# Performance work log

Hardware: AMD Instinct MI355X
Metric: run time of the kernel (lower is better)

## Reference

```python
import jax, jax.numpy as jnp
import numpy as np

B, N, IN, HID, OUT = 32, 128, 64, 128, 64
_off = np.ones((N, N)) - np.eye(N)
RECV, SEND = np.where(_off)  # rel_rec one-hot rows -> receiver idx, rel_send -> sender idx
E = N * (N - 1)


def _bn(x, g, b):
    # BatchNorm1d in training mode over flattened (B*M, C), eps=1e-5, biased var
    c = x.shape[-1]
    xf = x.reshape(-1, c)
    m = xf.mean(0)
    v = ((xf - m) ** 2).mean(0)
    return (((xf - m) / jnp.sqrt(v + 1e-5)) * g + b).reshape(x.shape)


def _mlp(x, W1, b1, W2, b2, g, b):
    h = jax.nn.silu(x @ W1 + b1)
    h = jax.nn.silu(h @ W2 + b2)
    return _bn(h, g, b)


def setup_inputs() -> dict:
    key = jax.random.key(0)
    ks = jax.random.split(key, 8)
    p = lambda k, s: jax.random.normal(k, s, dtype=jnp.float32) * 0.05
    return {
        "node_feature": jax.random.normal(ks[0], (B, N, IN), dtype=jnp.float32),
        "nodes_mask": jnp.ones((B, N), dtype=jnp.float32),
        "edges_mask": jnp.ones((B, E), dtype=jnp.float32),
        "eW1": p(ks[1], (2 * IN, HID)), "eb1": jnp.full((HID,), 0.1, jnp.float32),
        "eW2": p(ks[2], (HID, HID)), "eb2": jnp.full((HID,), 0.1, jnp.float32),
        "eg": jnp.ones((HID,), jnp.float32), "ebt": jnp.zeros((HID,), jnp.float32),
        "nW1": p(ks[3], (HID, HID)), "nb1": jnp.full((HID,), 0.1, jnp.float32),
        "nW2": p(ks[4], (HID, HID)), "nb2": jnp.full((HID,), 0.1, jnp.float32),
        "ng": jnp.ones((HID,), jnp.float32), "nbt": jnp.zeros((HID,), jnp.float32),
        "mW1": p(ks[5], (IN + HID, HID)), "mb1": jnp.full((HID,), 0.1, jnp.float32),
        "mW2": p(ks[6], (HID, OUT)), "mb2": jnp.full((OUT,), 0.1, jnp.float32),
        "mg": jnp.ones((OUT,), jnp.float32), "mbt": jnp.zeros((OUT,), jnp.float32),
        "t_nodes": 0, "t_edges": 0,
    }


def reference(node_feature, nodes_mask, edges_mask,
              eW1, eb1, eW2, eb2, eg, ebt,
              nW1, nb1, nW2, nb2, ng, nbt,
              mW1, mb1, mW2, mb2, mg, mbt,
              t_nodes, t_edges):
    # edge_model: rel_send/rel_rec one-hot matmuls == gathers
    senders = node_feature[:, SEND, :]    # [B,E,IN]
    receivers = node_feature[:, RECV, :]  # [B,E,IN]
    ef = jnp.concatenate([senders, receivers], axis=-1)  # [B,E,2*IN]
    # skip_first_edge_type=True, edge_types=2 -> only edge_nn[1], norm=1.0
    em = edges_mask[:, :, None]
    msg = _mlp(ef, eW1, eb1, eW2, eb2, eg, ebt) * em  # [B,E,HID]
    mij = msg / 1.0
    out = mij * em       # attention=False
    mij_m = mij * em
    # node_model: rel_rec.T matmul == scatter-sum over receivers, then / N
    incoming = jnp.zeros((B, N, HID), msg.dtype).at[:, RECV, :].add(out) / N
    incoming = _mlp(incoming, nW1, nb1, nW2, nb2, ng, nbt) * nodes_mask[:, :, None]
    nef = jnp.concatenate([node_feature, incoming], axis=-1)  # [B,N,IN+HID]
    out_node = _mlp(nef, mW1, mb1, mW2, mb2, mg, mbt) * nodes_mask[:, :, None]
    return (out_node, mij_m)
```

## Files before the change

kernel.cpp:

```cpp
#include <hip/hip_runtime.h>
#include <hip/hip_bf16.h>

#define BB    32
#define NNODE 128
#define INF   64
#define HIDF  128
#define OUTF  64
#define EE    (NNODE*(NNODE-1))
#define TILES 127
#define NBLK_EDGE (BB*TILES)
#define ROWS_E 520192.0f
#define ROWS_N 4096.0f
#define OUT0_ELEMS (BB*NNODE*OUTF)
#define H2_ELEMS ((size_t)520192*128)

typedef __bf16 bf16_t;
typedef __bf16 bfrag8 __attribute__((ext_vector_type(8)));
typedef __bf16 bfrag4 __attribute__((ext_vector_type(4)));
typedef float  floatx4 __attribute__((ext_vector_type(4)));

__device__ __forceinline__ float ld_g(const void* p, size_t i, int bf) {
    return bf ? (float)((const bf16_t*)p)[i] : ((const float*)p)[i];
}
__device__ __forceinline__ void st_g(void* p, size_t i, float v, int bf) {
    if (bf) ((bf16_t*)p)[i] = (bf16_t)v; else ((float*)p)[i] = v;
}
__device__ __forceinline__ void* mij_ptr(void* dout, int bf) {
    return bf ? (void*)((bf16_t*)dout + OUT0_ELEMS)
              : (void*)((float*)dout + OUT0_ELEMS);
}
__device__ __forceinline__ float silu_f(float x) {
    return x * __builtin_amdgcn_rcpf(1.0f + __expf(-x));
}

__device__ __forceinline__ int swz_col(int row, int col) {
    return col ^ ((row & 15) << 3);
}

__global__ void k_detect(const unsigned int* __restrict__ eg_words,
                         int* __restrict__ flag, float* __restrict__ totE)
{
    if (threadIdx.x == 0) *flag = (eg_words[0] == 0x3F803F80u) ? 1 : 0;
    if (threadIdx.x < 256) totE[threadIdx.x] = 0.f;
}

__global__ __launch_bounds__(256)
void k_prep(const void* __restrict__ W1g, const void* __restrict__ W2g,
            bf16_t* __restrict__ Wf1, bf16_t* __restrict__ Wf2,
            const int* __restrict__ flagp)
{
    const int bf  = *flagp;
    const int idx = blockIdx.x*256 + threadIdx.x;
    const int mat = idx >> 14;
    const int e   = idx & 16383;
    const int n   = e & 127, k = e >> 7;
    const float v = ld_g(mat ? W2g : W1g, e, bf);
    const int NB = n >> 4, ln = n & 15;
    const int ks = k >> 5, q = (k >> 3) & 3, j = k & 7;
    bf16_t* dst = mat ? Wf2 : Wf1;
    dst[((((NB*4 + ks)*4 + q)*16 + ln) << 3) + j] = (bf16_t)v;
}

__global__ __launch_bounds__(256, 4)
void k_edge_mlp(const void* __restrict__ nf,
                const bf16_t* __restrict__ Wf1, const void* __restrict__ b1g,
                const bf16_t* __restrict__ Wf2, const void* __restrict__ b2g,
                void* __restrict__ dout, bf16_t* __restrict__ h2ws,
                const int* __restrict__ flagp, float* __restrict__ totE,
                int h2mode)
{
    __shared__ __align__(16) bf16_t lA[128*128];
    __shared__ float sSum[128], sQ[128];
    const int bf  = *flagp;
    void* h2out = mij_ptr(dout, bf);
    const int bx   = blockIdx.x;
    const int bIdx = bx / TILES;
    const int t    = bx - bIdx*TILES;
    const int tid  = threadIdx.x;

    if (tid < 128) { sSum[tid] = 0.f; sQ[tid] = 0.f; }

    {
#pragma unroll
        for (int s = 0; s < 8; ++s) {
            const int u = tid + s*256;
            const int m = u >> 4;
            const int c = (u & 15) ^ (m & 15);
            const int eb = t*128 + m;
            const unsigned recv = ((unsigned)eb * 33027u) >> 22;
            const unsigned rr   = (unsigned)eb - recv*127u;
            const unsigned send = rr + (rr >= recv ? 1u : 0u);
            const int node = (c & 8) ? (int)recv : (int)send;
            const int coff = (c & 7) * 8;
            const size_t gi = ((size_t)(bIdx*NNODE + node))*INF + coff;
            if (bf) {
                ((uint4*)lA)[u] = *(const uint4*)((const bf16_t*)nf + gi);
            } else {
                const float4 f0 = *(const float4*)((const float*)nf + gi);
                const float4 f1 = *(const float4*)((const float*)nf + gi + 4);
                bfrag8 v;
                v[0]=(bf16_t)f0.x; v[1]=(bf16_t)f0.y; v[2]=(bf16_t)f0.z; v[3]=(bf16_t)f0.w;
                v[4]=(bf16_t)f1.x; v[5]=(bf16_t)f1.y; v[6]=(bf16_t)f1.z; v[7]=(bf16_t)f1.w;
                *(bfrag8*)(lA + (size_t)u*8) = v;
            }
        }
    }
    __syncthreads();

    const int w  = tid >> 6;
    const int L  = tid & 63;
    const int wr = w >> 1;
    const int wc = w & 1;
    const int q  = L >> 4;
    const int ln = L & 15;

    const floatx4 zero4 = {0.f, 0.f, 0.f, 0.f};
    floatx4 acc[4][4];
#pragma unroll
    for (int mt = 0; mt < 4; ++mt)
#pragma unroll
        for (int nt = 0; nt < 4; ++nt) acc[mt][nt] = zero4;

#pragma unroll
    for (int ks = 0; ks < 4; ++ks) {
        const int kk = ks*32;
        bfrag8 af[4], bv[4];
#pragma unroll
        for (int mt = 0; mt < 4; ++mt) {
            const int R = wr*64 + mt*16 + ln;
            af[mt] = *(const bfrag8*)(lA + R*128 + swz_col(R, kk + q*8));
        }
#pragma unroll
        for (int nt = 0; nt < 4; ++nt)
            bv[nt] = *(const bfrag8*)(Wf1 + ((size_t)((wc*4 + nt)*4 + ks)*64 + L)*8);
#pragma unroll
        for (int mt = 0; mt < 4; ++mt)
#pragma unroll
            for (int nt = 0; nt < 4; ++nt)
                acc[mt][nt] = __builtin_amdgcn_mfma_f32_16x16x32_bf16(
                    af[mt], bv[nt], acc[mt][nt], 0, 0, 0);
    }
    __syncthreads();

#pragma unroll
    for (int nt = 0; nt < 4; ++nt) {
        const int col = wc*64 + nt*16 + ln;
        const float bias = ld_g(b1g, col, bf);
#pragma unroll
        for (int mt = 0; mt < 4; ++mt)
#pragma unroll
            for (int r = 0; r < 4; ++r) {
                const int R = wr*64 + mt*16 + q*4 + r;
                lA[R*128 + swz_col(R, col)] = (bf16_t)silu_f(acc[mt][nt][r] + bias);
            }
    }
    __syncthreads();

#pragma unroll
    for (int mt = 0; mt < 4; ++mt)
#pragma unroll
        for (int nt = 0; nt < 4; ++nt) acc[mt][nt] = zero4;
#pragma unroll
    for (int ks = 0; ks < 4; ++ks) {
        const int kk = ks*32;
        bfrag8 af[4], bv[4];
#pragma unroll
        for (int mt = 0; mt < 4; ++mt) {
            const int R = wr*64 + mt*16 + ln;
            af[mt] = *(const bfrag8*)(lA + R*128 + swz_col(R, kk + q*8));
        }
#pragma unroll
        for (int nt = 0; nt < 4; ++nt)
            bv[nt] = *(const bfrag8*)(Wf2 + ((size_t)((wc*4 + nt)*4 + ks)*64 + L)*8);
#pragma unroll
        for (int mt = 0; mt < 4; ++mt)
#pragma unroll
            for (int nt = 0; nt < 4; ++nt)
                acc[mt][nt] = __builtin_amdgcn_mfma_f32_16x16x32_bf16(
                    af[mt], bv[nt], acc[mt][nt], 0, 0, 0);
    }
    __syncthreads();

#pragma unroll
    for (int nt = 0; nt < 4; ++nt) {
        const int col = wc*64 + nt*16 + ln;
        const float bias = ld_g(b2g, col, bf);
        float cs = 0.f, cq = 0.f;
#pragma unroll
        for (int mt = 0; mt < 4; ++mt)
#pragma unroll
            for (int r = 0; r < 4; ++r) {
                const int R = wr*64 + mt*16 + q*4 + r;
                const float v = silu_f(acc[mt][nt][r] + bias);
                cs += v; cq += v*v;
                lA[R*128 + swz_col(R, col)] = (bf16_t)v;
            }
        cs += __shfl_xor(cs, 16); cs += __shfl_xor(cs, 32);
        cq += __shfl_xor(cq, 16); cq += __shfl_xor(cq, 32);
        if (L < 16) { atomicAdd(&sSum[col], cs); atomicAdd(&sQ[col], cq); }
    }
    __syncthreads();

    {
        const size_t Rbase = ((size_t)bIdx*EE + (size_t)t*128) * 128;
#pragma unroll
        for (int s = 0; s < 8; ++s) {
            const int u = tid + s*256;
            const int m = u >> 4;
            const int c = (u & 15) ^ (m & 15);
            const size_t go = Rbase + (size_t)m*128 + c*8;
            if (h2mode) {
                *(uint4*)(h2ws + go) = ((const uint4*)lA)[u];
            } else if (bf) {
                *(uint4*)((bf16_t*)h2out + go) = ((const uint4*)lA)[u];
            } else {
                const bfrag8 vv = *(const bfrag8*)(lA + (size_t)u*8);
                float4 f0, f1;
                f0.x=(float)vv[0]; f0.y=(float)vv[1]; f0.z=(float)vv[2]; f0.w=(float)vv[3];
                f1.x=(float)vv[4]; f1.y=(float)vv[5]; f1.z=(float)vv[6]; f1.w=(float)vv[7];
                *(float4*)((float*)h2out + go)     = f0;
                *(float4*)((float*)h2out + go + 4) = f1;
            }
        }
        if (tid < 128) {
            atomicAdd(&totE[tid],       sSum[tid]);
            atomicAdd(&totE[128 + tid], sQ[tid]);
        }
    }
}

__global__ void k_finalize_edge(const float* __restrict__ tot,
                                const void* __restrict__ g,
                                const void* __restrict__ bt,
                                float* __restrict__ ab,
                                const int* __restrict__ flagp)
{
    const int bf = *flagp;
    const int c = threadIdx.x;
    const float m = tot[c] / ROWS_E;
    float v = tot[128 + c] / ROWS_E - m*m;
    v = fmaxf(v, 0.f);
    const float a = ld_g(g, c, bf) * rsqrtf(v + 1e-5f);
    ab[c]       = a;
    ab[128 + c] = ld_g(bt, c, bf) - m*a;
}

__global__ __launch_bounds__(256)
void k_bn_scatter(void* __restrict__ dout,
                  const bf16_t* __restrict__ h2ws,
                  const void* __restrict__ emask,
                  const float* __restrict__ ab,
                  float* __restrict__ inc,
                  const int* __restrict__ flagp, int h2mode)
{
    const int bf = *flagp;
    void* mij = mij_ptr(dout, bf);
    const void* h2 = h2mode ? (const void*)h2ws : (const void*)mij;
    const int h2bf = h2mode | bf;
    const int bx = blockIdx.x;
    const int b  = bx >> 7, i = bx & 127;
    const int tid = threadIdx.x;
    const int cg = tid & 15, p = tid >> 4;
    const int c0 = cg*8;
    float al[8], be[8];
#pragma unroll
    for (int j = 0; j < 8; ++j) { al[j] = ab[c0+j]; be[j] = ab[128+c0+j]; }
    const size_t seg = (size_t)b*EE + (size_t)i*127;
    float s[8];
#pragma unroll
    for (int j = 0; j < 8; ++j) s[j] = 0.f;
    for (int e = p; e < 127; e += 16) {
        const float em  = ld_g(emask, seg + e, bf);
        const float em2 = em*em;
        const size_t base = (seg + e)*128 + c0;
        float v[8];
        if (h2bf) {
            const bfrag8 u = *(const bfrag8*)((const bf16_t*)h2 + base);
#pragma unroll
            for (int j = 0; j < 8; ++j) v[j] = (float)u[j];
        } else {
            const float4 f0 = *(const float4*)((const float*)h2 + base);
            const float4 f1 = *(const float4*)((const float*)h2 + base + 4);
            v[0]=f0.x; v[1]=f0.y; v[2]=f0.z; v[3]=f0.w;
            v[4]=f1.x; v[5]=f1.y; v[6]=f1.z; v[7]=f1.w;
        }
#pragma unroll
        for (int j = 0; j < 8; ++j) { v[j] = (v[j]*al[j] + be[j])*em2; s[j] += v[j]; }
        if (bf) {
            bfrag8 u;
#pragma unroll
            for (int j = 0; j < 8; ++j) u[j] = (bf16_t)v[j];
            *(bfrag8*)((bf16_t*)mij + base) = u;
        } else {
            float4 f0, f1;
            f0.x=v[0]; f0.y=v[1]; f0.z=v[2]; f0.w=v[3];
            f1.x=v[4]; f1.y=v[5]; f1.z=v[6]; f1.w=v[7];
            *(float4*)((float*)mij + base)     = f0;
            *(float4*)((float*)mij + base + 4) = f1;
        }
    }
    __shared__ float sm[16][128];
#pragma unroll
    for (int j = 0; j < 8; ++j) sm[p][c0+j] = s[j];
    __syncthreads();
    if (tid < 128) {
        float tsum = 0.f;
#pragma unroll
        for (int wk = 0; wk < 16; ++wk) tsum += sm[wk][tid];
        inc[(size_t)(b*NNODE + i)*HIDF + tid] = tsum * (1.0f/NNODE);
    }
}

__global__ __launch_bounds__(128)
void k_node_mlp(const float* __restrict__ inc,
                const void* __restrict__ W1g, const void* __restrict__ b1g,
                const void* __restrict__ W2g, const void* __restrict__ b2g,
                float* __restrict__ h2n, float* __restrict__ partialN,
                const int* __restrict__ flagp)
{
    const int bf = *flagp;
    __shared__ float x[16][128];
    __shared__ float h[16][128];
    const int bx = blockIdx.x;
    const int tid = threadIdx.x;
    const int r0 = bx*16;
    for (int r = 0; r < 16; ++r) x[r][tid] = inc[(size_t)(r0 + r)*128 + tid];
    __syncthreads();

    float a1[16];
#pragma unroll
    for (int r = 0; r < 16; ++r) a1[r] = 0.f;
#pragma unroll 8
    for (int k = 0; k < 128; ++k) {
        const float wv = ld_g(W1g, k*128 + tid, bf);
#pragma unroll
        for (int r = 0; r < 16; ++r) a1[r] += x[r][k]*wv;
    }
    const float bias1 = ld_g(b1g, tid, bf);
#pragma unroll
    for (int r = 0; r < 16; ++r) h[r][tid] = silu_f(a1[r] + bias1);
    __syncthreads();

    float a2[16];
#pragma unroll
    for (int r = 0; r < 16; ++r) a2[r] = 0.f;
#pragma unroll 8
    for (int k = 0; k < 128; ++k) {
        const float wv = ld_g(W2g, k*128 + tid, bf);
#pragma unroll
        for (int r = 0; r < 16; ++r) a2[r] += h[r][k]*wv;
    }
    const float bias2 = ld_g(b2g, tid, bf);
    float s = 0.f, sq = 0.f;
#pragma unroll
    for (int r = 0; r < 16; ++r) {
        const float v = silu_f(a2[r] + bias2);
        h2n[(size_t)(r0 + r)*128 + tid] = v;
        s += v; sq += v*v;
    }
    partialN[(size_t)bx*256 + tid]       = s;
    partialN[(size_t)bx*256 + 128 + tid] = sq;
}

__global__ void k_finalize_node(const float* __restrict__ p,
                                const void* __restrict__ g,
                                const void* __restrict__ bt,
                                float* __restrict__ ab,
                                const int* __restrict__ flagp)
{
    const int bf = *flagp;
    const int c = threadIdx.x;
    float s = 0.f, qv = 0.f;
#pragma unroll 8
    for (int blk = 0; blk < 256; ++blk) { s += p[blk*256 + c]; qv += p[blk*256 + 128 + c]; }
    const float m = s / ROWS_N;
    float v = qv / ROWS_N - m*m;
    v = fmaxf(v, 0.f);
    const float a = ld_g(g, c, bf) * rsqrtf(v + 1e-5f);
    ab[c]       = a;
    ab[128 + c] = ld_g(bt, c, bf) - m*a;
}

__global__ __launch_bounds__(128)
void k_final_mlp(const void* __restrict__ nf,
                 const float* __restrict__ h2n, const float* __restrict__ abn,
                 const void* __restrict__ nmask,
                 const void* __restrict__ W1g, const void* __restrict__ b1g,
                 const void* __restrict__ W2g, const void* __restrict__ b2g,
                 float* __restrict__ hm, float* __restrict__ partialM,
                 const int* __restrict__ flagp)
{
    const int bf = *flagp;
    __shared__ float x[16][192];
    __shared__ float h[16][128];
    const int bx = blockIdx.x;
    const int tid = threadIdx.x;
    const int r0 = bx*16;
    const float an = abn[tid], bn = abn[128 + tid];
    for (int r = 0; r < 16; ++r) {
        const int row = r0 + r;
        const float mask = ld_g(nmask, row, bf);
        if (tid < 64) x[r][tid] = ld_g(nf, (size_t)row*INF + tid, bf);
        x[r][64 + tid] = (h2n[(size_t)row*128 + tid]*an + bn) * mask;
    }
    __syncthreads();

    float a1[16];
#pragma unroll
    for (int r = 0; r < 16; ++r) a1[r] = 0.f;
#pragma unroll 8
    for (int k = 0; k < 192; ++k) {
        const float wv = ld_g(W1g, k*128 + tid, bf);
#pragma unroll
        for (int r = 0; r < 16; ++r) a1[r] += x[r][k]*wv;
    }
    const float bias1 = ld_g(b1g, tid, bf);
#pragma unroll
    for (int r = 0; r < 16; ++r) h[r][tid] = silu_f(a1[r] + bias1);
    __syncthreads();

    if (tid < 64) {
        float a2[16];
#pragma unroll
        for (int r = 0; r < 16; ++r) a2[r] = 0.f;
#pragma unroll 8
        for (int k = 0; k < 128; ++k) {
            const float wv = ld_g(W2g, k*64 + tid, bf);
#pragma unroll
            for (int r = 0; r < 16; ++r) a2[r] += h[r][k]*wv;
        }
        const float bias2 = ld_g(b2g, tid, bf);
        float s = 0.f, sq = 0.f;
#pragma unroll
        for (int r = 0; r < 16; ++r) {
            const float v = silu_f(a2[r] + bias2);
            hm[(size_t)(r0 + r)*OUTF + tid] = v;
            s += v; sq += v*v;
        }
        partialM[(size_t)bx*128 + tid]      = s;
        partialM[(size_t)bx*128 + 64 + tid] = sq;
    }
}

__global__ void k_finalize_m(const float* __restrict__ p,
                             const void* __restrict__ g,
                             const void* __restrict__ bt,
                             float* __restrict__ ab,
                             const int* __restrict__ flagp)
{
    const int bf = *flagp;
    const int c = threadIdx.x;
    float s = 0.f, qv = 0.f;
#pragma unroll 8
    for (int blk = 0; blk < 256; ++blk) { s += p[blk*128 + c]; qv += p[blk*128 + 64 + c]; }
    const float m = s / ROWS_N;
    float v = qv / ROWS_N - m*m;
    v = fmaxf(v, 0.f);
    const float a = ld_g(g, c, bf) * rsqrtf(v + 1e-5f);
    ab[c]      = a;
    ab[64 + c] = ld_g(bt, c, bf) - m*a;
}

__global__ void k_out_node(const float* __restrict__ hm,
                           const float* __restrict__ abm,
                           const void* __restrict__ nmask,
                           void* __restrict__ dout,
                           const int* __restrict__ flagp)
{
    const int bf = *flagp;
    const int idx = blockIdx.x*256 + threadIdx.x;
    if (idx >= OUT0_ELEMS) return;
    const int c = idx & 63;
    const int row = idx >> 6;
    const float v = (hm[idx]*abm[c] + abm[64 + c]) * ld_g(nmask, row, bf);
    st_g(dout, idx, v, bf);
}

extern "C" void kernel_launch(void* const* d_in, const int* in_sizes, int n_in,
                              void* d_out, int out_size, void* d_ws, size_t ws_size,
                              hipStream_t stream)
{
    const void* nf    = d_in[0];
    const void* nmask = d_in[1];
    const void* emask = d_in[2];
    const void* eW1   = d_in[3];
    const void* eb1   = d_in[4];
    const void* eW2   = d_in[5];
    const void* eb2   = d_in[6];
    const void* eg    = d_in[7];
    const void* ebt   = d_in[8];
    const void* nW1   = d_in[9];
    const void* nb1   = d_in[10];
    const void* nW2   = d_in[11];
    const void* nb2   = d_in[12];
    const void* ng    = d_in[13];
    const void* nbt   = d_in[14];
    const void* mW1   = d_in[15];
    const void* mb1   = d_in[16];
    const void* mW2   = d_in[17];
    const void* mb2   = d_in[18];
    const void* mg    = d_in[19];
    const void* mbt   = d_in[20];

    float* W    = (float*)d_ws;
    int*   flag = (int*)W;
    float* totE = W    + 64;
    float* abE  = totE + 256;
    float* inc  = abE  + 256;
    float* h2n  = inc  + 524288;
    float* pN   = h2n  + 524288;
    float* abN  = pN   + 65536;
    float* hm   = abN  + 256;
    float* pM   = hm   + 262144;
    float* abM  = pM   + 32768;
    bf16_t* Wf1 = (bf16_t*)(abM + 128);
    bf16_t* Wf2 = Wf1 + 16384;
    bf16_t* h2ws = Wf2 + 16384;

    const size_t base_bytes = (size_t)((char*)h2ws - (char*)d_ws);
    const int h2mode = (ws_size >= base_bytes + H2_ELEMS*2 + 256) ? 1 : 0;

    k_detect<<<dim3(1), dim3(256), 0, stream>>>((const unsigned int*)eg, flag, totE);
    k_prep<<<dim3(128), dim3(256), 0, stream>>>(eW1, eW2, Wf1, Wf2, flag);
    k_edge_mlp<<<dim3(NBLK_EDGE), dim3(256), 0, stream>>>(nf, Wf1, eb1, Wf2, eb2, d_out, h2ws, flag, totE, h2mode);
    k_finalize_edge<<<dim3(1), dim3(128), 0, stream>>>(totE, eg, ebt, abE, flag);
    k_bn_scatter<<<dim3(BB*NNODE), dim3(256), 0, stream>>>(d_out, h2ws, emask, abE, inc, flag, h2mode);
    k_node_mlp<<<dim3(256), dim3(128), 0, stream>>>(inc, nW1, nb1, nW2, nb2, h2n, pN, flag);
    k_finalize_node<<<dim3(1), dim3(128), 0, stream>>>(pN, ng, nbt, abN, flag);
    k_final_mlp<<<dim3(256), dim3(128), 0, stream>>>(nf, h2n, abN, nmask, mW1, mb1, mW2, mb2, hm, pM, flag);
    k_finalize_m<<<dim3(1), dim3(64), 0, stream>>>(pM, mg, mbt, abM, flag);
    k_out_node<<<dim3(1024), dim3(256), 0, stream>>>(hm, abM, nmask, d_out, flag);
}
```

Before: 630.6 us.

## Factor first edge layer into per-node sender/receiver projections

```diff
diff --git a/kernel.cpp b/kernel.cpp
--- a/kernel.cpp
+++ b/kernel.cpp
@@ -16,7 +16,6 @@
 
 typedef __bf16 bf16_t;
 typedef __bf16 bfrag8 __attribute__((ext_vector_type(8)));
-typedef __bf16 bfrag4 __attribute__((ext_vector_type(4)));
 typedef float  floatx4 __attribute__((ext_vector_type(4)));
 
 __device__ __forceinline__ float ld_g(const void* p, size_t i, int bf) {
@@ -33,23 +32,24 @@
     return x * __builtin_amdgcn_rcpf(1.0f + __expf(-x));
 }
 
-__device__ __forceinline__ int swz_col(int row, int col) {
+__device__ __forceinline__ int swz_col(int row, int col)  {
     return col ^ ((row & 15) << 3);
 }
-
-__global__ void k_detect(const unsigned int* __restrict__ eg_words,
-                         int* __restrict__ flag, float* __restrict__ totE)
-{
-    if (threadIdx.x == 0) *flag = (eg_words[0] == 0x3F803F80u) ? 1 : 0;
-    if (threadIdx.x < 256) totE[threadIdx.x] = 0.f;
+__device__ __forceinline__ int swz64_col(int row, int col) {
+    return col ^ ((row & 7) << 3);
 }
 
 __global__ __launch_bounds__(256)
-void k_prep(const void* __restrict__ W1g, const void* __restrict__ W2g,
+void k_prep(const unsigned int* __restrict__ eg_words,
+            const void* __restrict__ W1g, const void* __restrict__ W2g,
             bf16_t* __restrict__ Wf1, bf16_t* __restrict__ Wf2,
-            const int* __restrict__ flagp)
-{
-    const int bf  = *flagp;
+            int* __restrict__ flag, float* __restrict__ totE)
+{
+    const int bf = (eg_words[0] == 0x3F803F80u) ? 1 : 0;
+    if (blockIdx.x == 0) {
+        if (threadIdx.x == 0) *flag = bf;
+        totE[threadIdx.x] = 0.f;
+    }
     const int idx = blockIdx.x*256 + threadIdx.x;
     const int mat = idx >> 14;
     const int e   = idx & 16383;
@@ -61,9 +61,91 @@
     dst[((((NB*4 + ks)*4 + q)*16 + ln) << 3) + j] = (bf16_t)v;
 }
 
+__global__ __launch_bounds__(256)
+void k_sr(const void* __restrict__ nf,
+          const bf16_t* __restrict__ Wf1, const void* __restrict__ b1g,
+          float* __restrict__ Sbuf, float* __restrict__ Rbuf,
+          const int* __restrict__ flagp)
+{
+    __shared__ __align__(16) bf16_t lA[128*64];
+    const int bf  = *flagp;
+    const int r0  = blockIdx.x * 128;
+    const int tid = threadIdx.x;
+
+#pragma unroll
+    for (int s = 0; s < 4; ++s) {
+        const int u = tid + s*256;
+        const int m = u >> 3;
+        const int c = (u & 7) ^ (m & 7);
+        const size_t gi = (size_t)(r0 + m)*INF + c*8;
+        if (bf) {
+            ((uint4*)lA)[u] = *(const uint4*)((const bf16_t*)nf + gi);
+        } else {
+            const float4 f0 = *(const float4*)((const float*)nf + gi);
+            const float4 f1 = *(const float4*)((const float*)nf + gi + 4);
+            bfrag8 v;
+            v[0]=(bf16_t)f0.x; v[1]=(bf16_t)f0.y; v[2]=(bf16_t)f0.z; v[3]=(bf16_t)f0.w;
+            v[4]=(bf16_t)f1.x; v[5]=(bf16_t)f1.y; v[6]=(bf16_t)f1.z; v[7]=(bf16_t)f1.w;
+            *(bfrag8*)(lA + (size_t)u*8) = v;
+        }
+    }
+    __syncthreads();
+
+    const int w  = tid >> 6;
+    const int L  = tid & 63;
+    const int wr = w >> 1;
+    const int wc = w & 1;
+    const int q  = L >> 4;
+    const int ln = L & 15;
+
+    const floatx4 zero4 = {0.f, 0.f, 0.f, 0.f};
+    floatx4 accS[4][4], accR[4][4];
+#pragma unroll
+    for (int mt = 0; mt < 4; ++mt)
+#pragma unroll
+        for (int nt = 0; nt < 4; ++nt) { accS[mt][nt] = zero4; accR[mt][nt] = zero4; }
+
+#pragma unroll
+    for (int ks = 0; ks < 2; ++ks) {
+        bfrag8 af[4], bs[4], br[4];
+#pragma unroll
+        for (int mt = 0; mt < 4; ++mt) {
+            const int Rr = wr*64 + mt*16 + ln;
+            af[mt] = *(const bfrag8*)(lA + Rr*64 + swz64_col(Rr, ks*32 + q*8));
+        }
+#pragma unroll
+        for (int nt = 0; nt < 4; ++nt) {
+            bs[nt] = *(const bfrag8*)(Wf1 + ((size_t)((wc*4 + nt)*4 + ks)*64 + L)*8);
+            br[nt] = *(const bfrag8*)(Wf1 + ((size_t)((wc*4 + nt)*4 + ks + 2)*64 + L)*8);
+        }
+#pragma unroll
+        for (int mt = 0; mt < 4; ++mt)
+#pragma unroll
+            for (int nt = 0; nt < 4; ++nt) {
+                accS[mt][nt] = __builtin_amdgcn_mfma_f32_16x16x32_bf16(
+                    af[mt], bs[nt], accS[mt][nt], 0, 0, 0);
+                accR[mt][nt] = __builtin_amdgcn_mfma_f32_16x16x32_bf16(
+                    af[mt], br[nt], accR[mt][nt], 0, 0, 0);
+            }
+    }
+
+#pragma unroll
+    for (int nt = 0; nt < 4; ++nt) {
+        const int col = wc*64 + nt*16 + ln;
+        const float bias = ld_g(b1g, col, bf);
+#pragma unroll
+        for (int mt = 0; mt < 4; ++mt)
+#pragma unroll
+            for (int r = 0; r < 4; ++r) {
+                const int row = wr*64 + mt*16 + q*4 + r;
+                Sbuf[(size_t)(r0 + row)*128 + col] = accS[mt][nt][r] + bias;
+                Rbuf[(size_t)(r0 + row)*128 + col] = accR[mt][nt][r];
+            }
+    }
+}
+
 __global__ __launch_bounds__(256, 4)
-void k_edge_mlp(const void* __restrict__ nf,
-                const bf16_t* __restrict__ Wf1, const void* __restrict__ b1g,
+void k_edge_mlp(const float* __restrict__ Sbuf, const float* __restrict__ Rbuf,
                 const bf16_t* __restrict__ Wf2, const void* __restrict__ b2g,
                 void* __restrict__ dout, bf16_t* __restrict__ h2ws,
                 const int* __restrict__ flagp, float* __restrict__ totE,
@@ -81,6 +163,7 @@
     if (tid < 128) { sSum[tid] = 0.f; sQ[tid] = 0.f; }
 
     {
+        const size_t nodeBase = (size_t)bIdx*NNODE*128;
 #pragma unroll
         for (int s = 0; s < 8; ++s) {
             const int u = tid + s*256;
@@ -90,19 +173,18 @@
             const unsigned recv = ((unsigned)eb * 33027u) >> 22;
             const unsigned rr   = (unsigned)eb - recv*127u;
             const unsigned send = rr + (rr >= recv ? 1u : 0u);
-            const int node = (c & 8) ? (int)recv : (int)send;
-            const int coff = (c & 7) * 8;
-            const size_t gi = ((size_t)(bIdx*NNODE + node))*INF + coff;
-            if (bf) {
-                ((uint4*)lA)[u] = *(const uint4*)((const bf16_t*)nf + gi);
-            } else {
-                const float4 f0 = *(const float4*)((const float*)nf + gi);
-                const float4 f1 = *(const float4*)((const float*)nf + gi + 4);
-                bfrag8 v;
-                v[0]=(bf16_t)f0.x; v[1]=(bf16_t)f0.y; v[2]=(bf16_t)f0.z; v[3]=(bf16_t)f0.w;
-                v[4]=(bf16_t)f1.x; v[5]=(bf16_t)f1.y; v[6]=(bf16_t)f1.z; v[7]=(bf16_t)f1.w;
-                *(bfrag8*)(lA + (size_t)u*8) = v;
-            }
+            const float* Sp = Sbuf + nodeBase + (size_t)send*128 + c*8;
+            const float* Rp = Rbuf + nodeBase + (size_t)recv*128 + c*8;
+            const float4 s0 = *(const float4*)Sp;
+            const float4 s1 = *(const float4*)(Sp + 4);
+            const float4 r0v = *(const float4*)Rp;
+            const float4 r1v = *(const float4*)(Rp + 4);
+            bfrag8 v;
+            v[0]=(bf16_t)silu_f(s0.x + r0v.x); v[1]=(bf16_t)silu_f(s0.y + r0v.y);
+            v[2]=(bf16_t)silu_f(s0.z + r0v.z); v[3]=(bf16_t)silu_f(s0.w + r0v.w);
+            v[4]=(bf16_t)silu_f(s1.x + r1v.x); v[5]=(bf16_t)silu_f(s1.y + r1v.y);
+            v[6]=(bf16_t)silu_f(s1.z + r1v.z); v[7]=(bf16_t)silu_f(s1.w + r1v.w);
+            *(bfrag8*)(lA + (size_t)u*8) = v;
         }
     }
     __syncthreads();
@@ -121,45 +203,6 @@
 #pragma unroll
         for (int nt = 0; nt < 4; ++nt) acc[mt][nt] = zero4;
 
-#pragma unroll
-    for (int ks = 0; ks < 4; ++ks) {
-        const int kk = ks*32;
-        bfrag8 af[4], bv[4];
-#pragma unroll
-        for (int mt = 0; mt < 4; ++mt) {
-            const int R = wr*64 + mt*16 + ln;
-            af[mt] = *(const bfrag8*)(lA + R*128 + swz_col(R, kk + q*8));
-        }
-#pragma unroll
-        for (int nt = 0; nt < 4; ++nt)
-            bv[nt] = *(const bfrag8*)(Wf1 + ((size_t)((wc*4 + nt)*4 + ks)*64 + L)*8);
-#pragma unroll
-        for (int mt = 0; mt < 4; ++mt)
-#pragma unroll
-            for (int nt = 0; nt < 4; ++nt)
-                acc[mt][nt] = __builtin_amdgcn_mfma_f32_16x16x32_bf16(
-                    af[mt], bv[nt], acc[mt][nt], 0, 0, 0);
-    }
-    __syncthreads();
-
-#pragma unroll
-    for (int nt = 0; nt < 4; ++nt) {
-        const int col = wc*64 + nt*16 + ln;
-        const float bias = ld_g(b1g, col, bf);
-#pragma unroll
-        for (int mt = 0; mt < 4; ++mt)
-#pragma unroll
-            for (int r = 0; r < 4; ++r) {
-                const int R = wr*64 + mt*16 + q*4 + r;
-                lA[R*128 + swz_col(R, col)] = (bf16_t)silu_f(acc[mt][nt][r] + bias);
-            }
-    }
-    __syncthreads();
-
-#pragma unroll
-    for (int mt = 0; mt < 4; ++mt)
-#pragma unroll
-        for (int nt = 0; nt < 4; ++nt) acc[mt][nt] = zero4;
 #pragma unroll
     for (int ks = 0; ks < 4; ++ks) {
         const int kk = ks*32;
@@ -229,27 +272,12 @@
     }
 }
 
-__global__ void k_finalize_edge(const float* __restrict__ tot,
-                                const void* __restrict__ g,
-                                const void* __restrict__ bt,
-                                float* __restrict__ ab,
-                                const int* __restrict__ flagp)
-{
-    const int bf = *flagp;
-    const int c = threadIdx.x;
-    const float m = tot[c] / ROWS_E;
-    float v = tot[128 + c] / ROWS_E - m*m;
-    v = fmaxf(v, 0.f);
-    const float a = ld_g(g, c, bf) * rsqrtf(v + 1e-5f);
-    ab[c]       = a;
-    ab[128 + c] = ld_g(bt, c, bf) - m*a;
-}
-
 __global__ __launch_bounds__(256)
 void k_bn_scatter(void* __restrict__ dout,
                   const bf16_t* __restrict__ h2ws,
                   const void* __restrict__ emask,
-                  const float* __restrict__ ab,
+                  const float* __restrict__ totE,
+                  const void* __restrict__ g, const void* __restrict__ bt,
                   float* __restrict__ inc,
                   const int* __restrict__ flagp, int h2mode)
 {
@@ -264,7 +292,14 @@
     const int c0 = cg*8;
     float al[8], be[8];
 #pragma unroll
-    for (int j = 0; j < 8; ++j) { al[j] = ab[c0+j]; be[j] = ab[128+c0+j]; }
+    for (int j = 0; j < 8; ++j) {
+        const int c = c0 + j;
+        const float mn = totE[c] * (1.0f/ROWS_E);
+        float vr = totE[128 + c] * (1.0f/ROWS_E) - mn*mn;
+        vr = fmaxf(vr, 0.f);
+        al[j] = ld_g(g, c, bf) * rsqrtf(vr + 1e-5f);
+        be[j] = ld_g(bt, c, bf) - mn*al[j];
+    }
     const size_t seg = (size_t)b*EE + (size_t)i*127;
     float s[8];
 #pragma unroll
@@ -515,16 +550,17 @@
     float* abM  = pM   + 32768;
     bf16_t* Wf1 = (bf16_t*)(abM + 128);
     bf16_t* Wf2 = Wf1 + 16384;
-    bf16_t* h2ws = Wf2 + 16384;
+    float* Sbuf = (float*)(Wf2 + 16384);
+    float* Rbuf = Sbuf + 524288;
+    bf16_t* h2ws = (bf16_t*)(Rbuf + 524288);
 
     const size_t base_bytes = (size_t)((char*)h2ws - (char*)d_ws);
     const int h2mode = (ws_size >= base_bytes + H2_ELEMS*2 + 256) ? 1 : 0;
 
-    k_detect<<<dim3(1), dim3(256), 0, stream>>>((const unsigned int*)eg, flag, totE);
-    k_prep<<<dim3(128), dim3(256), 0, stream>>>(eW1, eW2, Wf1, Wf2, flag);
-    k_edge_mlp<<<dim3(NBLK_EDGE), dim3(256), 0, stream>>>(nf, Wf1, eb1, Wf2, eb2, d_out, h2ws, flag, totE, h2mode);
-    k_finalize_edge<<<dim3(1), dim3(128), 0, stream>>>(totE, eg, ebt, abE, flag);
-    k_bn_scatter<<<dim3(BB*NNODE), dim3(256), 0, stream>>>(d_out, h2ws, emask, abE, inc, flag, h2mode);
+    k_prep<<<dim3(128), dim3(256), 0, stream>>>((const unsigned int*)eg, eW1, eW2, Wf1, Wf2, flag, totE);
+    k_sr<<<dim3(32), dim3(256), 0, stream>>>(nf, Wf1, eb1, Sbuf, Rbuf, flag);
+    k_edge_mlp<<<dim3(NBLK_EDGE), dim3(256), 0, stream>>>(Sbuf, Rbuf, Wf2, eb2, d_out, h2ws, flag, totE, h2mode);
+    k_bn_scatter<<<dim3(BB*NNODE), dim3(256), 0, stream>>>(d_out, h2ws, emask, totE, eg, ebt, inc, flag, h2mode);
     k_node_mlp<<<dim3(256), dim3(128), 0, stream>>>(inc, nW1, nb1, nW2, nb2, h2n, pN, flag);
     k_finalize_node<<<dim3(1), dim3(128), 0, stream>>>(pN, ng, nbt, abN, flag);
     k_final_mlp<<<dim3(256), dim3(128), 0, stream>>>(nf, h2n, abN, nmask, mW1, mb1, mW2, mb2, hm, pM, flag);
```

Measured after the change: 616.4 us. -2.2%, faster.
